# Kernel tuning notes

Hardware: AMD Instinct MI355X
Metric: run time of the kernel (lower is better)

The kernel has to match this reference:

```python
import jax, jax.numpy as jnp
import numpy as np

N, C, G, H = 262144, 512, 16, 16   # nodes, channels, groups, half_group_c
GH = G * H                          # 256
CH_HID = 64                         # channel_mlp hidden = max(GH//4, 8)
SP_HID = 8                          # space_mlp hidden = max(H//4, 8)
B = 1024                            # number of graphs
TEMP = 1.0
EPS = 1e-5


def setup_inputs() -> dict:
    k = jax.random.key(0)
    ks = jax.random.split(k, 20)
    s = 0.02
    rn = lambda kk, sh: jax.random.normal(kk, sh, dtype=jnp.float32)
    return {
        "x": rn(ks[0], (N, C)),
        "batch": jnp.sort(jax.random.randint(ks[1], (N,), 0, B, dtype=jnp.int32)),
        "num_segments": B,
        "cweight": s * rn(ks[2], (1, H)),
        "cbias": 1.0 + s * rn(ks[3], (1, H)),
        "sweight": s * rn(ks[4], (1, H)),
        "sbias": 1.0 + s * rn(ks[5], (1, H)),
        "ch_W1": rn(ks[6], (2 * GH, CH_HID)) / np.sqrt(2 * GH),
        "ch_b1": s * rn(ks[7], (CH_HID,)),
        "ch_W2": rn(ks[8], (CH_HID, GH)) / np.sqrt(CH_HID),
        "ch_b2": s * rn(ks[9], (GH,)),
        "gn_weight": 1.0 + s * rn(ks[10], (GH,)),
        "gn_bias": s * rn(ks[11], (GH,)),
        "sp_W1": rn(ks[12], (3 * H, SP_HID)) / np.sqrt(3 * H),
        "sp_b1": s * rn(ks[13], (SP_HID,)),
        "sp_W2": rn(ks[14], (SP_HID, H)) / np.sqrt(SP_HID),
        "sp_b2": s * rn(ks[15], (H,)),
        "init_scale": jnp.float32(0.1),
        "gnorm_weight": 1.0 + s * rn(ks[16], (C,)),
        "gnorm_bias": s * rn(ks[17], (C,)),
        "gnorm_mean_scale": 1.0 + s * rn(ks[18], (C,)),
    }


def reference(x, batch, num_segments, cweight, cbias, sweight, sbias,
              ch_W1, ch_b1, ch_W2, ch_b2, gn_weight, gn_bias,
              sp_W1, sp_b1, sp_W2, sp_b2, init_scale,
              gnorm_weight, gnorm_bias, gnorm_mean_scale):
    n = x.shape[0]
    xg = x.reshape(n, G, 2 * H)
    x_c = xg[:, :, :H]                      # [N, G, H] channel branch
    x_s = xg[:, :, H:]                      # [N, G, H] spatial branch
    xcf = x_c.reshape(n, GH)

    # --- segment mean / max pooling over graphs ---
    cnt = jax.ops.segment_sum(jnp.ones((n,), x.dtype), batch, num_segments)  # [B]
    gap_mean = jax.ops.segment_sum(xcf, batch, num_segments) / jnp.maximum(cnt, 1.0)[:, None]
    gap_max = jax.ops.segment_max(xcf, batch, num_segments)
    gap_max = jnp.where(cnt[:, None] > 0, gap_max, 0.0)    # empty graphs -> 0
    gap_cat = jnp.concatenate([gap_mean, gap_max], axis=1)  # [B, 2*GH]

    # --- channel gate MLP ---
    hch = jax.nn.relu(gap_cat @ ch_W1 + ch_b1)
    ch_gate = jax.nn.sigmoid((hch @ ch_W2 + ch_b2).reshape(-1, G, H) / TEMP)
    ch_gate = ch_gate * (1.0 + cweight.reshape(1, 1, H)) + cbias.reshape(1, 1, H)
    x_c = x_c * ch_gate[batch]

    # --- GroupNorm over each group's H channels (spatial extent 1) ---
    mu = x_s.mean(axis=2, keepdims=True)
    var = ((x_s - mu) ** 2).mean(axis=2, keepdims=True)
    xn = (x_s - mu) / jnp.sqrt(var + EPS)
    xn = xn * gn_weight.reshape(1, G, H) + gn_bias.reshape(1, G, H)

    # --- spatial context across groups (std is unbiased, ddof=1) ---
    mean_ctx = xn.mean(axis=1)
    max_ctx = xn.max(axis=1)
    std_ctx = jnp.sqrt(((xn - mean_ctx[:, None, :]) ** 2).sum(axis=1) / (G - 1))
    sc = jnp.concatenate([mean_ctx, max_ctx, std_ctx], axis=-1)  # [N, 3H]
    hs = jax.nn.relu(sc @ sp_W1 + sp_b1)
    sp_gate = jax.nn.sigmoid((hs @ sp_W2 + sp_b2).reshape(n, 1, H) / TEMP)
    sp_gate = sp_gate * (1.0 + sweight.reshape(1, 1, H)) + sbias.reshape(1, 1, H)
    x_s = x_s * sp_gate

    # stack -> [N,G,H,2] -> permute -> [N,G,2,H] -> [N,C]
    out = jnp.stack([x_c, x_s], axis=-1).transpose(0, 1, 3, 2).reshape(n, C)
    out = out + jnp.tanh(init_scale) * x

    # --- GraphNorm (PyG): per-graph, per-channel ---
    inv_cnt = 1.0 / jnp.maximum(cnt, 1.0)[:, None]
    gmean = jax.ops.segment_sum(out, batch, num_segments) * inv_cnt
    outc = out - gmean[batch] * gnorm_mean_scale
    gvar = jax.ops.segment_sum(outc * outc, batch, num_segments) * inv_cnt
    out = gnorm_weight * outc / jnp.sqrt(gvar + EPS)[batch] + gnorm_bias

    # channel shuffle with groups=2
    return out.reshape(n, 2, C // 2).transpose(0, 2, 1).reshape(n, C)
```

## Files before the change

kernel.cpp:

```cpp
#include <hip/hip_runtime.h>
#include <hip/hip_bf16.h>
#include <math.h>

#define NN 262144
#define CC 512
#define BB 1024
#define EPSF 1e-5f

typedef float f32x4 __attribute__((ext_vector_type(4)));

__device__ __forceinline__ int lower_bound_i(const int* __restrict__ a, int n, int v) {
    int lo = 0, hi = n;
    while (lo < hi) { int mid = (lo + hi) >> 1; if (a[mid] < v) lo = mid + 1; else hi = mid; }
    return lo;
}

__device__ __forceinline__ float sigmoidf(float v) { return 1.0f / (1.0f + __expf(-v)); }

template<int CTRL>
__device__ __forceinline__ float dppAdd(float v) {
    int t = __builtin_amdgcn_update_dpp(0, __float_as_int(v), CTRL, 0xf, 0xf, true);
    return v + __int_as_float(t);
}
template<int CTRL>
__device__ __forceinline__ float dppMax(float v) {
    int t = __builtin_amdgcn_update_dpp(0, __float_as_int(v), CTRL, 0xf, 0xf, true);
    return fmaxf(v, __int_as_float(t));
}

__global__ void kA(const float* __restrict__ x, const int* __restrict__ batch,
                   const float* __restrict__ sweight, const float* __restrict__ sbias,
                   const float* __restrict__ gn_w, const float* __restrict__ gn_b,
                   const float* __restrict__ sp_W1, const float* __restrict__ sp_b1,
                   const float* __restrict__ sp_W2, const float* __restrict__ sp_b2,
                   const float* __restrict__ init_scale,
                   float* __restrict__ segS1, float* __restrict__ segMx,
                   float* __restrict__ segS2, float* __restrict__ segT1,
                   float* __restrict__ segT2, int* __restrict__ segCnt,
                   float* __restrict__ spgt)
{
    const int b    = blockIdx.x;
    const int tid  = threadIdx.x;
    const int lane = tid & 63;
    const int w    = tid >> 6;
    const int g    = lane & 15;
    const int q    = lane >> 4;
    const int h0   = q * 4;
    const int kk   = g & 7;

    __shared__ float red[4][5][256];

    const int s = lower_bound_i(batch, NN, b);
    const int e = lower_bound_i(batch, NN, b + 1);
    const float tau = tanhf(init_scale[0]);

    float gwv[4], gbv[4], b2v[4], swv[4], sbv[4], w1m[4], w1x[4], w1s[4], w2r[4];
#pragma unroll
    for (int j = 0; j < 4; ++j) {
        const int h = h0 + j;
        gwv[j] = gn_w[g * 16 + h];
        gbv[j] = gn_b[g * 16 + h];
        b2v[j] = sp_b2[h];
        swv[j] = sweight[h];
        sbv[j] = sbias[h];
        w1m[j] = sp_W1[h * 8 + kk];
        w1x[j] = sp_W1[(16 + h) * 8 + kk];
        w1s[j] = sp_W1[(32 + h) * 8 + kk];
        w2r[j] = sp_W2[kk * 16 + h];
    }
    const float b1k = sp_b1[kk];

    float sc1[4] = {0.f,0.f,0.f,0.f}, sc2[4] = {0.f,0.f,0.f,0.f};
    float st1[4] = {0.f,0.f,0.f,0.f}, st2[4] = {0.f,0.f,0.f,0.f};
    float mxc[4] = {-INFINITY,-INFINITY,-INFINITY,-INFINITY};

    int n0 = s + 2 * w;
    int n1 = 0; bool v1 = false;
    float4 c40, s40, c41, s41;
    if (n0 < e) {
        n1 = (n0 + 1 < e) ? n0 + 1 : e - 1;
        v1 = (n0 + 1 < e);
        const float* r0 = x + (size_t)n0 * CC + g * 32 + h0;
        const float* r1 = x + (size_t)n1 * CC + g * 32 + h0;
        c40 = *(const float4*)r0;  s40 = *(const float4*)(r0 + 16);
        c41 = *(const float4*)r1;  s41 = *(const float4*)(r1 + 16);
    }

    while (n0 < e) {
        const int m0 = n0 + 8;
        int m1 = 0; bool mv1 = false;
        float4 nc0, ns0, nc1, ns1;
        if (m0 < e) {
            m1 = (m0 + 1 < e) ? m0 + 1 : e - 1;
            mv1 = (m0 + 1 < e);
            const float* r0 = x + (size_t)m0 * CC + g * 32 + h0;
            const float* r1 = x + (size_t)m1 * CC + g * 32 + h0;
            nc0 = *(const float4*)r0;  ns0 = *(const float4*)(r0 + 16);
            nc1 = *(const float4*)r1;  ns1 = *(const float4*)(r1 + 16);
        }

        {
            const float c0[4] = {c40.x, c40.y, c40.z, c40.w};
#pragma unroll
            for (int j = 0; j < 4; ++j) {
                sc1[j] += c0[j];
                sc2[j] = fmaf(c0[j], c0[j], sc2[j]);
                mxc[j] = fmaxf(mxc[j], c0[j]);
            }
        }
        if (v1) {
            const float c1[4] = {c41.x, c41.y, c41.z, c41.w};
#pragma unroll
            for (int j = 0; j < 4; ++j) {
                sc1[j] += c1[j];
                sc2[j] = fmaf(c1[j], c1[j], sc2[j]);
                mxc[j] = fmaxf(mxc[j], c1[j]);
            }
        }

        float sa[2][4], spg[2][4];
        sa[0][0] = s40.x; sa[0][1] = s40.y; sa[0][2] = s40.z; sa[0][3] = s40.w;
        sa[1][0] = s41.x; sa[1][1] = s41.y; sa[1][2] = s41.z; sa[1][3] = s41.w;

        float ls[2], lq[2];
#pragma unroll
        for (int rr = 0; rr < 2; ++rr) {
            ls[rr] = sa[rr][0] + sa[rr][1] + sa[rr][2] + sa[rr][3];
            lq[rr] = fmaf(sa[rr][0], sa[rr][0], fmaf(sa[rr][1], sa[rr][1],
                     fmaf(sa[rr][2], sa[rr][2], sa[rr][3] * sa[rr][3])));
        }
#pragma unroll
        for (int rr = 0; rr < 2; ++rr) {
            ls[rr] += __shfl_xor(ls[rr], 16); ls[rr] += __shfl_xor(ls[rr], 32);
            lq[rr] += __shfl_xor(lq[rr], 16); lq[rr] += __shfl_xor(lq[rr], 32);
        }
        float xn[2][4];
#pragma unroll
        for (int rr = 0; rr < 2; ++rr) {
            const float mu   = ls[rr] * 0.0625f;
            const float var  = lq[rr] * 0.0625f - mu * mu;
            const float rstd = rsqrtf(var + EPSF);
#pragma unroll
            for (int j = 0; j < 4; ++j)
                xn[rr][j] = fmaf((sa[rr][j] - mu) * rstd, gwv[j], gbv[j]);
        }

        float sm[2][4], s2c[2][4], mx[2][4];
#pragma unroll
        for (int rr = 0; rr < 2; ++rr) {
#pragma unroll
            for (int j = 0; j < 4; ++j) {
                float v = xn[rr][j];
                v = dppAdd<0xB1>(v); v = dppAdd<0x4E>(v);
                v = dppAdd<0x124>(v); v = dppAdd<0x128>(v);
                sm[rr][j] = v;
                float u = xn[rr][j] * xn[rr][j];
                u = dppAdd<0xB1>(u); u = dppAdd<0x4E>(u);
                u = dppAdd<0x124>(u); u = dppAdd<0x128>(u);
                s2c[rr][j] = u;
                float m = xn[rr][j];
                m = dppMax<0xB1>(m); m = dppMax<0x4E>(m);
                m = dppMax<0x124>(m); m = dppMax<0x128>(m);
                mx[rr][j] = m;
            }
        }

        float p[2] = {0.f, 0.f};
#pragma unroll
        for (int rr = 0; rr < 2; ++rr) {
#pragma unroll
            for (int j = 0; j < 4; ++j) {
                const float mean = sm[rr][j] * 0.0625f;
                const float ss   = fmaxf(s2c[rr][j] - 16.0f * mean * mean, 0.0f);
                const float stdc = sqrtf(ss * (1.0f / 15.0f));
                p[rr] = fmaf(mean, w1m[j], p[rr]);
                p[rr] = fmaf(mx[rr][j], w1x[j], p[rr]);
                p[rr] = fmaf(stdc, w1s[j], p[rr]);
            }
        }
#pragma unroll
        for (int rr = 0; rr < 2; ++rr) {
            p[rr] += __shfl_xor(p[rr], 16); p[rr] += __shfl_xor(p[rr], 32);
        }
#pragma unroll
        for (int rr = 0; rr < 2; ++rr) {
            const float hsk = fmaxf(p[rr] + b1k, 0.0f);
#pragma unroll
            for (int j = 0; j < 4; ++j) {
                float t = hsk * w2r[j];
                t = dppAdd<0xB1>(t); t = dppAdd<0x4E>(t); t = dppAdd<0x141>(t);
                spg[rr][j] = fmaf(sigmoidf(t + b2v[j]), 1.0f + swv[j], sbv[j]) + tau;
            }
        }

#pragma unroll
        for (int j = 0; j < 4; ++j) {
            const float os0 = spg[0][j] * sa[0][j];
            st1[j] += os0;
            st2[j] = fmaf(os0, os0, st2[j]);
        }
        if (g == 0)
            *(float4*)(spgt + (size_t)n0 * 16 + h0) =
                make_float4(spg[0][0], spg[0][1], spg[0][2], spg[0][3]);
        if (v1) {
#pragma unroll
            for (int j = 0; j < 4; ++j) {
                const float os1 = spg[1][j] * sa[1][j];
                st1[j] += os1;
                st2[j] = fmaf(os1, os1, st2[j]);
            }
            if (g == 0)
                *(float4*)(spgt + (size_t)n1 * 16 + h0) =
                    make_float4(spg[1][0], spg[1][1], spg[1][2], spg[1][3]);
        }

        n0 = m0; n1 = m1; v1 = mv1;
        c40 = nc0; s40 = ns0; c41 = nc1; s41 = ns1;
    }

    const int ch = g * 16 + h0;
    *(float4*)&red[w][0][ch] = make_float4(sc1[0], sc1[1], sc1[2], sc1[3]);
    *(float4*)&red[w][1][ch] = make_float4(mxc[0], mxc[1], mxc[2], mxc[3]);
    *(float4*)&red[w][2][ch] = make_float4(sc2[0], sc2[1], sc2[2], sc2[3]);
    *(float4*)&red[w][3][ch] = make_float4(st1[0], st1[1], st1[2], st1[3]);
    *(float4*)&red[w][4][ch] = make_float4(st2[0], st2[1], st2[2], st2[3]);
    __syncthreads();
    if (tid < 256) {
        const int c = tid;
        float a0 = red[0][0][c] + red[1][0][c] + red[2][0][c] + red[3][0][c];
        float a1 = fmaxf(fmaxf(red[0][1][c], red[1][1][c]), fmaxf(red[2][1][c], red[3][1][c]));
        float a2 = red[0][2][c] + red[1][2][c] + red[2][2][c] + red[3][2][c];
        float a3 = red[0][3][c] + red[1][3][c] + red[2][3][c] + red[3][3][c];
        float a4 = red[0][4][c] + red[1][4][c] + red[2][4][c] + red[3][4][c];
        segS1[b * 256 + c] = a0;
        segMx[b * 256 + c] = a1;
        segS2[b * 256 + c] = a2;
        segT1[b * 256 + c] = a3;
        segT2[b * 256 + c] = a4;
    }
    if (tid == 0) segCnt[b] = e - s;
}

__global__ void kF(const float* __restrict__ segS1, const float* __restrict__ segMx,
                   const float* __restrict__ segS2, const float* __restrict__ segT1,
                   const float* __restrict__ segT2, const int* __restrict__ segCnt,
                   const float* __restrict__ ch_W1, const float* __restrict__ ch_b1,
                   const float* __restrict__ ch_W2, const float* __restrict__ ch_b2,
                   const float* __restrict__ cweight, const float* __restrict__ cbias,
                   const float* __restrict__ init_scale,
                   const float* __restrict__ gms, const float* __restrict__ gw,
                   const float* __restrict__ gb,
                   float* __restrict__ coef, float* __restrict__ offs)
{
    const int b = blockIdx.x;
    const int tid = threadIdx.x;
    __shared__ float gap[512];
    __shared__ float hch[64];
    __shared__ float part[4][64];

    const int cnt = segCnt[b];
    const float inv = 1.0f / (float)max(cnt, 1);
    if (tid < 256) {
        gap[tid] = segS1[b * 256 + tid] * inv;
        const float m = segMx[b * 256 + tid];
        gap[256 + tid] = (cnt > 0) ? m : 0.0f;
    }
    __syncthreads();
    {
        const int t = tid & 63, pp = tid >> 6;
        float acc = 0.f;
        for (int i = pp * 128; i < pp * 128 + 128; ++i)
            acc = fmaf(gap[i], ch_W1[i * 64 + t], acc);
        part[pp][t] = acc;
    }
    __syncthreads();
    if (tid < 64)
        hch[tid] = fmaxf(part[0][tid] + part[1][tid] + part[2][tid] + part[3][tid] + ch_b1[tid], 0.0f);
    __syncthreads();
    if (tid < 256) {
        const int c = tid, gg = c >> 4, h = c & 15;
        float acc = ch_b2[c];
        for (int k = 0; k < 64; ++k) acc = fmaf(hch[k], ch_W2[k * 256 + c], acc);
        const float chg = fmaf(sigmoidf(acc), 1.0f + cweight[h], cbias[h]);
        const float tau = tanhf(init_scale[0]);
        const float ct = chg + tau;
        const int colc = gg * 32 + h, cols = colc + 16;
        {
            const float S1 = segS1[b * 256 + c], S2 = segS2[b * 256 + c];
            const float m  = ct * S1 * inv;
            const float e2 = ct * ct * S2 * inv;
            const float smv = gms[colc];
            const float gv = fmaxf(e2 - m * m * smv * (2.0f - smv), 0.0f);
            const float A  = gw[colc] * rsqrtf(gv + EPSF);
            coef[b * 512 + colc] = A * ct;
            offs[b * 512 + colc] = gb[colc] - m * smv * A;
        }
        {
            const float T1 = segT1[b * 256 + c], T2 = segT2[b * 256 + c];
            const float m  = T1 * inv;
            const float e2 = T2 * inv;
            const float smv = gms[cols];
            const float gv = fmaxf(e2 - m * m * smv * (2.0f - smv), 0.0f);
            const float A  = gw[cols] * rsqrtf(gv + EPSF);
            coef[b * 512 + cols] = A;
            offs[b * 512 + cols] = gb[cols] - m * smv * A;
        }
    }
}

__global__ void kB(const float* __restrict__ x, const int* __restrict__ batch,
                   const float* __restrict__ coef, const float* __restrict__ offs,
                   const float* __restrict__ spgt, float* __restrict__ out)
{
    const int b = BB - 1 - blockIdx.x;
    const int tid = threadIdx.x;
    const int lane = tid & 63, w = tid >> 6;
    const int l2 = lane * 2;
    const int p0 = (lane >> 3) & 1;

    const int s = lower_bound_i(batch, NN, b);
    const int e = lower_bound_i(batch, NN, b + 1);

    const float* cfb = coef + (size_t)b * 512;
    const float* ofb = offs + (size_t)b * 512;
    const float cf0 = cfb[l2],       cf1 = cfb[l2 + 1];
    const float cf2 = cfb[128 + l2], cf3 = cfb[129 + l2];
    const float cf4 = cfb[256 + l2], cf5 = cfb[257 + l2];
    const float cf6 = cfb[384 + l2], cf7 = cfb[385 + l2];
    const float of0 = ofb[l2],       of1 = ofb[l2 + 1];
    const float of2 = ofb[128 + l2], of3 = ofb[129 + l2];
    const float of4 = ofb[256 + l2], of5 = ofb[257 + l2];
    const float of6 = ofb[384 + l2], of7 = ofb[385 + l2];

    for (int n0 = s + 2 * w; n0 < e; n0 += 8) {
        const int n1 = (n0 + 1 < e) ? n0 + 1 : e - 1;
        const bool v1 = (n0 + 1 < e);

        const float2* r0 = (const float2*)(x + (size_t)n0 * CC);
        const float2* r1 = (const float2*)(x + (size_t)n1 * CC);
        const float2 xa[2] = { r0[lane],        r1[lane] };
        const float2 xb[2] = { r0[64 + lane],   r1[64 + lane] };
        const float2 xc[2] = { r0[128 + lane],  r1[128 + lane] };
        const float2 xd[2] = { r0[192 + lane],  r1[192 + lane] };
        const float2 sp[2] = {
            *(const float2*)(spgt + (size_t)n0 * 16 + (l2 & 15)),
            *(const float2*)(spgt + (size_t)n1 * 16 + (l2 & 15)) };

#pragma unroll
        for (int rr = 0; rr < 2; ++rr) {
            if (rr == 1 && !v1) break;
            const float me = p0 ? sp[rr].x : 1.0f;
            const float mo = p0 ? sp[rr].y : 1.0f;

            const float v0 = fmaf(cf0 * me, xa[rr].x, of0);
            const float v1f = fmaf(cf1 * mo, xa[rr].y, of1);
            const float v2 = fmaf(cf2 * me, xb[rr].x, of2);
            const float v3 = fmaf(cf3 * mo, xb[rr].y, of3);
            const float v4 = fmaf(cf4 * me, xc[rr].x, of4);
            const float v5 = fmaf(cf5 * mo, xc[rr].y, of5);
            const float v6 = fmaf(cf6 * me, xd[rr].x, of6);
            const float v7 = fmaf(cf7 * mo, xd[rr].y, of7);

            f32x4* o4 = (f32x4*)(out + (size_t)(rr ? n1 : n0) * CC);
            f32x4 pa = {v0, v4, v1f, v5};
            f32x4 pb = {v2, v6, v3, v7};
            __builtin_nontemporal_store(pa, &o4[lane]);
            __builtin_nontemporal_store(pb, &o4[64 + lane]);
        }
    }
}

extern "C" void kernel_launch(void* const* d_in, const int* in_sizes, int n_in,
                              void* d_out, int out_size, void* d_ws, size_t ws_size,
                              hipStream_t stream) {
    (void)in_sizes; (void)n_in; (void)out_size; (void)ws_size;
    const float* x        = (const float*)d_in[0];
    const int*   batch    = (const int*)d_in[1];
    const float* cweight  = (const float*)d_in[3];
    const float* cbias    = (const float*)d_in[4];
    const float* sweight  = (const float*)d_in[5];
    const float* sbias    = (const float*)d_in[6];
    const float* ch_W1    = (const float*)d_in[7];
    const float* ch_b1    = (const float*)d_in[8];
    const float* ch_W2    = (const float*)d_in[9];
    const float* ch_b2    = (const float*)d_in[10];
    const float* gn_w     = (const float*)d_in[11];
    const float* gn_b     = (const float*)d_in[12];
    const float* sp_W1    = (const float*)d_in[13];
    const float* sp_b1    = (const float*)d_in[14];
    const float* sp_W2    = (const float*)d_in[15];
    const float* sp_b2    = (const float*)d_in[16];
    const float* init_sc  = (const float*)d_in[17];
    const float* gnw      = (const float*)d_in[18];
    const float* gnb      = (const float*)d_in[19];
    const float* gms      = (const float*)d_in[20];

    float* ws    = (float*)d_ws;
    float* segS1 = ws;
    float* segMx = segS1 + BB * 256;
    float* segS2 = segMx + BB * 256;
    float* segT1 = segS2 + BB * 256;
    float* segT2 = segT1 + BB * 256;
    int*   segCnt = (int*)(segT2 + BB * 256);
    float* coef  = (float*)(segCnt + BB);
    float* offs  = coef + BB * 512;
    float* spgt  = offs + BB * 512;
    float* outp  = (float*)d_out;

    kA<<<BB, 256, 0, stream>>>(x, batch, sweight, sbias, gn_w, gn_b,
                               sp_W1, sp_b1, sp_W2, sp_b2, init_sc,
                               segS1, segMx, segS2, segT1, segT2, segCnt, spgt);
    kF<<<BB, 256, 0, stream>>>(segS1, segMx, segS2, segT1, segT2, segCnt,
                               ch_W1, ch_b1, ch_W2, ch_b2, cweight, cbias,
                               init_sc, gms, gnw, gnb, coef, offs);
    kB<<<BB, 256, 0, stream>>>(x, batch, coef, offs, spgt, outp);
}
```

Measured before the change: 459.5 us.

## Fuse per-graph MLP into stats kernel and split apply kernel blocks per graph

Folds the per-graph channel MLP and GraphNorm coefficient computation (formerly a separate kernel) into the tail of the statistics kernel, passing the segment sums through shared memory. This drops one launch and the global round trip of the segment-statistic buffers. The apply kernel now launches two blocks per graph, each handling half of that graph's nodes, to raise parallelism and occupancy. The price is extra shared memory in the stats kernel and a duplicated pair of binary searches per apply block.

```diff
diff --git a/kernel.cpp b/kernel.cpp
--- a/kernel.cpp
+++ b/kernel.cpp
@@ -34,9 +34,12 @@
                    const float* __restrict__ sp_W1, const float* __restrict__ sp_b1,
                    const float* __restrict__ sp_W2, const float* __restrict__ sp_b2,
                    const float* __restrict__ init_scale,
-                   float* __restrict__ segS1, float* __restrict__ segMx,
-                   float* __restrict__ segS2, float* __restrict__ segT1,
-                   float* __restrict__ segT2, int* __restrict__ segCnt,
+                   const float* __restrict__ ch_W1, const float* __restrict__ ch_b1,
+                   const float* __restrict__ ch_W2, const float* __restrict__ ch_b2,
+                   const float* __restrict__ cweight, const float* __restrict__ cbias,
+                   const float* __restrict__ gms, const float* __restrict__ gw,
+                   const float* __restrict__ gb,
+                   float* __restrict__ coef, float* __restrict__ offs,
                    float* __restrict__ spgt)
 {
     const int b    = blockIdx.x;
@@ -49,9 +52,14 @@
     const int kk   = g & 7;
 
     __shared__ float red[4][5][256];
+    __shared__ float gap[512];
+    __shared__ float part[4][64];
+    __shared__ float hch[64];
+    __shared__ float sS1[256], sS2[256], sT1[256], sT2[256];
 
     const int s = lower_bound_i(batch, NN, b);
     const int e = lower_bound_i(batch, NN, b + 1);
+    const int cnt = e - s;
     const float tau = tanhf(init_scale[0]);
 
     float gwv[4], gbv[4], b2v[4], swv[4], sbv[4], w1m[4], w1x[4], w1s[4], w2r[4];
@@ -225,47 +233,20 @@
     *(float4*)&red[w][3][ch] = make_float4(st1[0], st1[1], st1[2], st1[3]);
     *(float4*)&red[w][4][ch] = make_float4(st2[0], st2[1], st2[2], st2[3]);
     __syncthreads();
-    if (tid < 256) {
+    const float inv = 1.0f / (float)max(cnt, 1);
+    {
         const int c = tid;
         float a0 = red[0][0][c] + red[1][0][c] + red[2][0][c] + red[3][0][c];
         float a1 = fmaxf(fmaxf(red[0][1][c], red[1][1][c]), fmaxf(red[2][1][c], red[3][1][c]));
         float a2 = red[0][2][c] + red[1][2][c] + red[2][2][c] + red[3][2][c];
         float a3 = red[0][3][c] + red[1][3][c] + red[2][3][c] + red[3][3][c];
         float a4 = red[0][4][c] + red[1][4][c] + red[2][4][c] + red[3][4][c];
-        segS1[b * 256 + c] = a0;
-        segMx[b * 256 + c] = a1;
-        segS2[b * 256 + c] = a2;
-        segT1[b * 256 + c] = a3;
-        segT2[b * 256 + c] = a4;
-    }
-    if (tid == 0) segCnt[b] = e - s;
-}
-
-__global__ void kF(const float* __restrict__ segS1, const float* __restrict__ segMx,
-                   const float* __restrict__ segS2, const float* __restrict__ segT1,
-                   const float* __restrict__ segT2, const int* __restrict__ segCnt,
-                   const float* __restrict__ ch_W1, const float* __restrict__ ch_b1,
-                   const float* __restrict__ ch_W2, const float* __restrict__ ch_b2,
-                   const float* __restrict__ cweight, const float* __restrict__ cbias,
-                   const float* __restrict__ init_scale,
-                   const float* __restrict__ gms, const float* __restrict__ gw,
-                   const float* __restrict__ gb,
-                   float* __restrict__ coef, float* __restrict__ offs)
-{
-    const int b = blockIdx.x;
-    const int tid = threadIdx.x;
-    __shared__ float gap[512];
-    __shared__ float hch[64];
-    __shared__ float part[4][64];
-
-    const int cnt = segCnt[b];
-    const float inv = 1.0f / (float)max(cnt, 1);
-    if (tid < 256) {
-        gap[tid] = segS1[b * 256 + tid] * inv;
-        const float m = segMx[b * 256 + tid];
-        gap[256 + tid] = (cnt > 0) ? m : 0.0f;
+        sS1[c] = a0; sS2[c] = a2; sT1[c] = a3; sT2[c] = a4;
+        gap[c] = a0 * inv;
+        gap[256 + c] = (cnt > 0) ? a1 : 0.0f;
     }
     __syncthreads();
+
     {
         const int t = tid & 63, pp = tid >> 6;
         float acc = 0.f;
@@ -277,16 +258,15 @@
     if (tid < 64)
         hch[tid] = fmaxf(part[0][tid] + part[1][tid] + part[2][tid] + part[3][tid] + ch_b1[tid], 0.0f);
     __syncthreads();
-    if (tid < 256) {
+    {
         const int c = tid, gg = c >> 4, h = c & 15;
         float acc = ch_b2[c];
         for (int k = 0; k < 64; ++k) acc = fmaf(hch[k], ch_W2[k * 256 + c], acc);
         const float chg = fmaf(sigmoidf(acc), 1.0f + cweight[h], cbias[h]);
-        const float tau = tanhf(init_scale[0]);
         const float ct = chg + tau;
         const int colc = gg * 32 + h, cols = colc + 16;
         {
-            const float S1 = segS1[b * 256 + c], S2 = segS2[b * 256 + c];
+            const float S1 = sS1[c], S2 = sS2[c];
             const float m  = ct * S1 * inv;
             const float e2 = ct * ct * S2 * inv;
             const float smv = gms[colc];
@@ -296,7 +276,7 @@
             offs[b * 512 + colc] = gb[colc] - m * smv * A;
         }
         {
-            const float T1 = segT1[b * 256 + c], T2 = segT2[b * 256 + c];
+            const float T1 = sT1[c], T2 = sT2[c];
             const float m  = T1 * inv;
             const float e2 = T2 * inv;
             const float smv = gms[cols];
@@ -312,14 +292,19 @@
                    const float* __restrict__ coef, const float* __restrict__ offs,
                    const float* __restrict__ spgt, float* __restrict__ out)
 {
-    const int b = BB - 1 - blockIdx.x;
+    const int bb   = blockIdx.x >> 1;
+    const int half = blockIdx.x & 1;
+    const int b    = BB - 1 - bb;
     const int tid = threadIdx.x;
     const int lane = tid & 63, w = tid >> 6;
     const int l2 = lane * 2;
     const int p0 = (lane >> 3) & 1;
 
-    const int s = lower_bound_i(batch, NN, b);
-    const int e = lower_bound_i(batch, NN, b + 1);
+    const int s0 = lower_bound_i(batch, NN, b);
+    const int e0 = lower_bound_i(batch, NN, b + 1);
+    const int mid = s0 + ((e0 - s0 + 1) >> 1);
+    const int s = half ? mid : s0;
+    const int e = half ? e0 : mid;
 
     const float* cfb = coef + (size_t)b * 512;
     const float* ofb = offs + (size_t)b * 512;
@@ -396,22 +381,14 @@
     const float* gms      = (const float*)d_in[20];
 
     float* ws    = (float*)d_ws;
-    float* segS1 = ws;
-    float* segMx = segS1 + BB * 256;
-    float* segS2 = segMx + BB * 256;
-    float* segT1 = segS2 + BB * 256;
-    float* segT2 = segT1 + BB * 256;
-    int*   segCnt = (int*)(segT2 + BB * 256);
-    float* coef  = (float*)(segCnt + BB);
+    float* coef  = ws;
     float* offs  = coef + BB * 512;
     float* spgt  = offs + BB * 512;
     float* outp  = (float*)d_out;
 
     kA<<<BB, 256, 0, stream>>>(x, batch, sweight, sbias, gn_w, gn_b,
                                sp_W1, sp_b1, sp_W2, sp_b2, init_sc,
-                               segS1, segMx, segS2, segT1, segT2, segCnt, spgt);
-    kF<<<BB, 256, 0, stream>>>(segS1, segMx, segS2, segT1, segT2, segCnt,
                                ch_W1, ch_b1, ch_W2, ch_b2, cweight, cbias,
-                               init_sc, gms, gnw, gnb, coef, offs);
-    kB<<<BB, 256, 0, stream>>>(x, batch, coef, offs, spgt, outp);
-}
+                               gms, gnw, gnb, coef, offs, spgt);
+    kB<<<BB * 2, 256, 0, stream>>>(x, batch, coef, offs, spgt, outp);
+}
```

Result: faster. 407.2 us (-11.4%).
